# Optimization experiments

Hardware: AMD Instinct MI355X
Metric: run time of the kernel (lower is better)

The kernel has to match this reference:

```python
import jax, jax.numpy as jnp
import numpy as np

FILTER = [1.0, 3.0, 3.0, 1.0]
FILTER_RADIUS = len(FILTER) // 2  # = 2


def setup_inputs() -> dict:
    key = jax.random.key(0)
    x = jax.random.normal(key, (16, 128, 128, 128), dtype=jnp.float32)
    # CreateLowpassKernel(Filter, Inplace=True): outer product of the 1-D taps, normalized.
    w = np.array([FILTER], dtype=np.float32)  # [1, 4]
    k = w.T @ w                               # [4, 4]
    kernel = jnp.asarray(k / k.sum(), dtype=jnp.float32)
    return {"x": x, "kernel": kernel}


def pixel_shuffle(x, r):
    # [B, C*r*r, H, W] -> [B, C, H*r, W*r] (torch pixel_shuffle semantics)
    B, C, H, W = x.shape
    c = C // (r * r)
    x = x.reshape(B, c, r, r, H, W)
    x = x.transpose(0, 1, 4, 2, 5, 3)  # B, c, H, r, W, r
    return x.reshape(B, c, H * r, W * r)


def reference(x, kernel):
    # pixel_shuffle by 2, then upfirdn2d(up=1, down=1, padding=FilterRadius):
    # pad by FilterRadius on all sides and apply the 2-D FIR filter as a true
    # convolution (kernel flipped), depthwise across channels.
    x = pixel_shuffle(x, 2)                      # [B, C, 2H, 2W]
    B, C, H, W = x.shape
    f = jnp.flip(kernel, (0, 1))                 # true convolution -> flip taps
    w = jnp.tile(f[None, None], (C, 1, 1, 1))    # [C, 1, kh, kw] depthwise
    p = FILTER_RADIUS
    return jax.lax.conv_general_dilated(
        x, w, window_strides=(1, 1), padding=[(p, p), (p, p)],
        dimension_numbers=("NCHW", "OIHW", "NCHW"),
        feature_group_count=C)  # [B, C, 2H+1, 2W+1]
```

## Files before the change

kernel.cpp:

```cpp
#include <hip/hip_runtime.h>

constexpr int Hn = 128;
constexpr int Wn = 128;
constexpr int SH = 2 * Hn;
constexpr int OH = SH + 1;
constexpr int OW = 257;
constexpr int HW = Hn * Wn;
constexpr int TY = 65;
constexpr int NSTRIP = 4;
constexpr int NBC = 16 * 32;
constexpr int PF = 4;
constexpr int NIT = TY + 3;

__global__ __launch_bounds__(256, 8) void upsamp_fir_lds(
    const float* __restrict__ x,
    const float* __restrict__ k4,
    float* __restrict__ out)
{
    const int tix = threadIdx.x;
    const int bc  = blockIdx.x;
    const int oh0 = blockIdx.y * TY;
    const float* xp = x + (size_t)bc * 4 * HW;

    float fh[4], fv[4];
#pragma unroll
    for (int j = 0; j < 4; ++j) fh[j] = k4[j] + k4[4+j] + k4[8+j] + k4[12+j];
#pragma unroll
    for (int i = 0; i < 4; ++i) fv[i] = k4[4*i] + k4[4*i+1] + k4[4*i+2] + k4[4*i+3];
    const float h0 = fh[3], h1 = fh[2], h2 = fh[1], h3 = fh[0];
    const float g0 = fv[3], g1 = fv[2], g2 = fv[1], g3 = fv[0];

    __shared__ float lds[2][2][132];
    if (tix < 8) {
        int b = tix >> 2, r = tix & 3;
        lds[b][r >> 1][(r & 1) ? 129 : 0] = 0.f;
    }

    const int eo       = tix < 128 ? 0 : 1;
    const int lane     = tix & 127;
    const int stageIdx = 1 + lane;

    auto xload = [&](int s) -> float {
        return xp[(size_t)(2 * (s & 1) + eo) * HW + (size_t)(s >> 1) * Wn + lane];
    };

    const int c    = tix;
    const int mi   = c >> 1;
    const int codd = c & 1;
    const bool edge = (tix == 255);

    float* const obase = out + (size_t)bc * OH * OW;

    float rr0 = 0, rr1 = 0, rr2 = 0, rr3 = 0;
    { int s = oh0 - 2; if ((unsigned)s < (unsigned)SH) rr0 = xload(s); }
    { int s = oh0 - 1; if ((unsigned)s < (unsigned)SH) rr1 = xload(s); }
    { int s = oh0;     if ((unsigned)s < (unsigned)SH) rr2 = xload(s); }
    { int s = oh0 + 1; if ((unsigned)s < (unsigned)SH) rr3 = xload(s); }

    float hm3 = 0, hm2 = 0, hm1 = 0;
    float em3 = 0, em2 = 0, em1 = 0;

    auto step = [&](int m, float& rr, int buf) {
        const int s = oh0 - 2 + m;
        lds[buf][eo][stageIdx] = rr;
        float nv = 0.f;
        const int sp = s + PF;
        if (m < NIT - PF && sp < SH) nv = xload(sp);
        rr = nv;
        __syncthreads();
        const float* EB = lds[buf][0];
        const float* OB = lds[buf][1];
        const float* P = codd ? (OB + mi) : (EB + mi);
        const float* Q = codd ? (EB + mi + 1) : (OB + mi);
        const float p0 = P[0], p1 = P[1];
        const float q0 = Q[0], q1 = Q[1];
        const float hn = h0*p0 + h1*q0 + h2*p1 + h3*q1;
        float en = 0.f;
        if (edge) {
            en = h0*EB[128] + h1*OB[128] + h2*EB[129] + h3*OB[129];
        }
        if (m >= 3) {
            const int oh = oh0 + m - 3;
            if (oh < OH) {
                float* p = obase + (size_t)oh * OW;
                p[c] = g0*hm3 + g1*hm2 + g2*hm1 + g3*hn;
                if (edge) p[256] = g0*em3 + g1*em2 + g2*em1 + g3*en;
            }
        }
        hm3 = hm2; hm2 = hm1; hm1 = hn;
        em3 = em2; em2 = em1; em1 = en;
    };

    for (int mm = 0; mm < NIT; mm += 4) {
        step(mm + 0, rr0, 0);
        step(mm + 1, rr1, 1);
        step(mm + 2, rr2, 0);
        step(mm + 3, rr3, 1);
    }
}

extern "C" void kernel_launch(void* const* d_in, const int* in_sizes, int n_in,
                              void* d_out, int out_size, void* d_ws, size_t ws_size,
                              hipStream_t stream)
{
    const float* x  = (const float*)d_in[0];
    const float* k4 = (const float*)d_in[1];
    float* out      = (float*)d_out;

    dim3 grid(NBC, NSTRIP, 1);
    upsamp_fir_lds<<<grid, dim3(256), 0, stream>>>(x, k4, out);
}
```

Baseline: 249.0 us.

## Replace LDS row staging with per-wavefront strips using shuffles and float2 loads

Each 64-lane wavefront now handles its own strip of 17 output rows and computes 4 output columns per lane. Neighbouring inputs come from cross-lane shuffles with float2 loads, instead of staging rows in shared memory behind a block-wide barrier on every row. This removes the LDS traffic and the per-row __syncthreads, at the cost of more halo rows being reloaded across strips. Stores become 4 consecutive floats per lane in rows of odd width 257, so they are unaligned, and the explicit prefetch distance is shortened to 2 rows.

```diff
diff --git a/kernel.cpp b/kernel.cpp
--- a/kernel.cpp
+++ b/kernel.cpp
@@ -6,20 +6,23 @@
 constexpr int OH = SH + 1;
 constexpr int OW = 257;
 constexpr int HW = Hn * Wn;
-constexpr int TY = 65;
-constexpr int NSTRIP = 4;
+constexpr int TY = 17;
+constexpr int NSTRIP = 16;
 constexpr int NBC = 16 * 32;
-constexpr int PF = 4;
 constexpr int NIT = TY + 3;
 
-__global__ __launch_bounds__(256, 8) void upsamp_fir_lds(
+__global__ __launch_bounds__(256, 8) void upsamp_fir_wave(
     const float* __restrict__ x,
     const float* __restrict__ k4,
     float* __restrict__ out)
 {
-    const int tix = threadIdx.x;
-    const int bc  = blockIdx.x;
-    const int oh0 = blockIdx.y * TY;
+    const int tix   = threadIdx.x;
+    const int lane  = tix & 63;
+    const int wid   = tix >> 6;
+    const int bc    = blockIdx.x;
+    const int strip = blockIdx.y * 4 + wid;
+    const int oh0   = strip * TY;
+
     const float* xp = x + (size_t)bc * 4 * HW;
 
     float fh[4], fv[4];
@@ -30,72 +33,64 @@
     const float h0 = fh[3], h1 = fh[2], h2 = fh[1], h3 = fh[0];
     const float g0 = fv[3], g1 = fv[2], g2 = fv[1], g3 = fv[0];
 
-    __shared__ float lds[2][2][132];
-    if (tix < 8) {
-        int b = tix >> 2, r = tix & 3;
-        lds[b][r >> 1][(r & 1) ? 129 : 0] = 0.f;
-    }
+    const bool l0  = (lane == 0);
+    const bool l63 = (lane == 63);
+    const int  colOff = 2 * lane;
 
-    const int eo       = tix < 128 ? 0 : 1;
-    const int lane     = tix & 127;
-    const int stageIdx = 1 + lane;
-
-    auto xload = [&](int s) -> float {
-        return xp[(size_t)(2 * (s & 1) + eo) * HW + (size_t)(s >> 1) * Wn + lane];
+    auto loadrow = [&](int s, float2& e2, float2& o2) {
+        if ((unsigned)s >= (unsigned)SH) {
+            e2 = make_float2(0.f, 0.f); o2 = e2; return;
+        }
+        const float* be = xp + (size_t)((s & 1) * 2) * HW
+                             + (size_t)(s >> 1) * Wn + colOff;
+        e2 = *(const float2*)be;
+        o2 = *(const float2*)(be + HW);
     };
 
-    const int c    = tix;
-    const int mi   = c >> 1;
-    const int codd = c & 1;
-    const bool edge = (tix == 255);
+    float2 eA, oA, eB, oB;
+    loadrow(oh0 - 2, eA, oA);
+    loadrow(oh0 - 1, eB, oB);
+
+    float m30=0,m31=0,m32=0,m33=0;
+    float m20=0,m21=0,m22=0,m23=0;
+    float m10=0,m11=0,m12=0,m13=0;
+    float e3=0, e2r=0, e1r=0;
 
     float* const obase = out + (size_t)bc * OH * OW;
 
-    float rr0 = 0, rr1 = 0, rr2 = 0, rr3 = 0;
-    { int s = oh0 - 2; if ((unsigned)s < (unsigned)SH) rr0 = xload(s); }
-    { int s = oh0 - 1; if ((unsigned)s < (unsigned)SH) rr1 = xload(s); }
-    { int s = oh0;     if ((unsigned)s < (unsigned)SH) rr2 = xload(s); }
-    { int s = oh0 + 1; if ((unsigned)s < (unsigned)SH) rr3 = xload(s); }
-
-    float hm3 = 0, hm2 = 0, hm1 = 0;
-    float em3 = 0, em2 = 0, em1 = 0;
-
-    auto step = [&](int m, float& rr, int buf) {
-        const int s = oh0 - 2 + m;
-        lds[buf][eo][stageIdx] = rr;
-        float nv = 0.f;
-        const int sp = s + PF;
-        if (m < NIT - PF && sp < SH) nv = xload(sp);
-        rr = nv;
-        __syncthreads();
-        const float* EB = lds[buf][0];
-        const float* OB = lds[buf][1];
-        const float* P = codd ? (OB + mi) : (EB + mi);
-        const float* Q = codd ? (EB + mi + 1) : (OB + mi);
-        const float p0 = P[0], p1 = P[1];
-        const float q0 = Q[0], q1 = Q[1];
-        const float hn = h0*p0 + h1*q0 + h2*p1 + h3*q1;
-        float en = 0.f;
-        if (edge) {
-            en = h0*EB[128] + h1*OB[128] + h2*EB[129] + h3*OB[129];
-        }
-        if (m >= 3) {
-            const int oh = oh0 + m - 3;
+    auto step = [&](int i, float2& E2, float2& O2) {
+        const int s = oh0 - 2 + i;
+        const float Ex = E2.x, Ey = E2.y, Ox = O2.x, Oy = O2.y;
+        float Em1 = __shfl_up(Ey, 1);   Em1 = l0  ? 0.f : Em1;
+        float Om1 = __shfl_up(Oy, 1);   Om1 = l0  ? 0.f : Om1;
+        float Ep1 = __shfl_down(Ex, 1); Ep1 = l63 ? 0.f : Ep1;
+        const float H0 = h0*Em1 + h1*Om1 + h2*Ex + h3*Ox;
+        const float H1 = h0*Om1 + h1*Ex  + h2*Ox + h3*Ey;
+        const float H2 = h0*Ex  + h1*Ox  + h2*Ey + h3*Oy;
+        const float H3 = h0*Ox  + h1*Ey  + h2*Oy + h3*Ep1;
+        const float H4 = h0*Ey  + h1*Oy;
+        if (i + 2 < NIT) loadrow(s + 2, E2, O2);
+        if (i >= 3) {
+            const int oh = oh0 + i - 3;
             if (oh < OH) {
-                float* p = obase + (size_t)oh * OW;
-                p[c] = g0*hm3 + g1*hm2 + g2*hm1 + g3*hn;
-                if (edge) p[256] = g0*em3 + g1*em2 + g2*em1 + g3*en;
+                float* pr = obase + (size_t)oh * OW + 4 * lane;
+                pr[0] = g0*m30 + g1*m20 + g2*m10 + g3*H0;
+                pr[1] = g0*m31 + g1*m21 + g2*m11 + g3*H1;
+                pr[2] = g0*m32 + g1*m22 + g2*m12 + g3*H2;
+                pr[3] = g0*m33 + g1*m23 + g2*m13 + g3*H3;
+                if (l63) pr[4] = g0*e3 + g1*e2r + g2*e1r + g3*H4;
             }
         }
-        hm3 = hm2; hm2 = hm1; hm1 = hn;
-        em3 = em2; em2 = em1; em1 = en;
+        m30=m20; m31=m21; m32=m22; m33=m23;
+        m20=m10; m21=m11; m22=m12; m23=m13;
+        m10=H0;  m11=H1;  m12=H2;  m13=H3;
+        e3=e2r;  e2r=e1r; e1r=H4;
     };
 
-    for (int mm = 0; mm < NIT; mm += 4) {
-        step(mm + 0, rr0, 0);
-        step(mm + 1, rr1, 1);
-        step(mm + 2, rr2, 0);
-        step(mm + 3, rr3, 1);
+#pragma unroll
+    for (int i = 0; i < NIT; i += 2) {
+        step(i,     eA, oA);
+        step(i + 1, eB, oB);
     }
 }
 
@@ -107,6 +102,6 @@
     const float* k4 = (const float*)d_in[1];
     float* out      = (float*)d_out;
 
-    dim3 grid(NBC, NSTRIP, 1);
-    upsamp_fir_lds<<<grid, dim3(256), 0, stream>>>(x, k4, out);
+    dim3 grid(NBC, NSTRIP / 4, 1);
+    upsamp_fir_wave<<<grid, dim3(256), 0, stream>>>(x, k4, out);
 }
```

Measured after the change: 291.6 us. 1.17x slower.
